# Kernel optimization log

Measured on AMD Instinct MI355X. Metric: run time of the kernel, lower is better.

The kernel has to match this reference:

```python
import jax, jax.numpy as jnp
import numpy as np

DIMENSIONS = 10000
NUM_LEVELS = 100
SIZE = 617
NUM_CLASSES = 26
BATCH = 32


def setup_inputs() -> dict:
    key = jax.random.key(0)
    k1, k2, k3 = jax.random.split(key, 3)
    x = jax.random.uniform(k1, (BATCH, SIZE), dtype=jnp.float32)  # values in [0,1]
    # Random embedding: bipolar {-1,+1} hypervectors
    id_weight = jnp.where(jax.random.uniform(k2, (SIZE, DIMENSIONS)) > 0.5, 1.0, -1.0).astype(jnp.float32)
    # Level embedding: bipolar hypervectors per quantization level
    level_weight = jnp.where(jax.random.uniform(k3, (NUM_LEVELS, DIMENSIONS)) > 0.5, 1.0, -1.0).astype(jnp.float32)
    classify_weight = jnp.zeros((NUM_CLASSES, DIMENSIONS), dtype=jnp.float32)
    return {"x": x, "id_weight": id_weight, "level_weight": level_weight, "classify_weight": classify_weight}


def reference(x, id_weight, level_weight, classify_weight):
    # Level embedding: map continuous values in [low=0, high=1] to level indices
    idx = jnp.clip(jnp.round(x * (NUM_LEVELS - 1)), 0, NUM_LEVELS - 1).astype(jnp.int32)  # (B, S)
    value_hv = level_weight[idx]                     # gather -> (B, S, D)
    bound = id_weight[None, :, :] * value_hv         # bind (elementwise multiply)
    multiset = jnp.sum(bound, axis=1)                # sum over feature axis -> (B, D)
    enc = jnp.where(multiset > 0, 1.0, -1.0)         # hard_quantize
    logit = jnp.einsum('bd,cd->bc', enc, classify_weight)  # Linear, no bias
    return logit
```

## Files before the change

### kernel.cpp

```cpp
#include <hip/hip_runtime.h>

typedef unsigned int u32;
typedef unsigned char u8;
typedef unsigned long long u64;

#define DIMS   10000
#define LEVELS 100
#define SSIZE  617
#define SPAD   624
#define NCLS   26
#define BATCH  32
#define WORDS  313
#define WPITCH 320
#define DPITCH 10240
#define NTILE  5
#define NCH    13
#define CHUNK  48
#define SOPITCH 640

#define OFF_OFFT 0x000000u
#define OFF_IDB  0x020000u
#define OFF_LVB  0x100000u
#define OFF_P8   0x140000u
#define SLOT_BYTES ((size_t)BATCH * DPITCH)

#define PK_ROWS (SPAD + LEVELS + 1)

__global__ __launch_bounds__(256) void k_pack(const float* __restrict__ x,
                                              const float* __restrict__ idw,
                                              const float* __restrict__ lvw,
                                              u32* __restrict__ idb,
                                              u32* __restrict__ lvb,
                                              u32* __restrict__ offt,
                                              float* __restrict__ out)
{
    const int g = blockIdx.x;
    const int r = blockIdx.y;
    const int t = threadIdx.x;
    const bool isLvl = r >= SPAD;
    const int rl = r - SPAD;
    const int d0 = g * 1024 + 4 * t;

    u32 nib = 0;
    const bool rowValid = isLvl ? (rl < LEVELS) : (r < SSIZE);
    if (d0 + 3 < DIMS && rowValid) {
        const float* src = isLvl ? (lvw + (size_t)rl * DIMS)
                                 : (idw + (size_t)r * DIMS);
        float4 f = *(const float4*)(src + d0);
        nib =  (__builtin_bit_cast(u32, f.x) >> 31)
            | ((__builtin_bit_cast(u32, f.y) >> 31) << 1)
            | ((__builtin_bit_cast(u32, f.z) >> 31) << 2)
            | ((__builtin_bit_cast(u32, f.w) >> 31) << 3);
    }
    __shared__ u32 nibs[256];
    nibs[t] = nib;
    __syncthreads();
    if (t < 32) {
        u32 w = 0;
#pragma unroll
        for (int j = 0; j < 8; ++j) w |= nibs[t * 8 + j] << (4 * j);
        u32* dst = isLvl ? (lvb + (size_t)rl * WPITCH)
                         : (idb + (size_t)r * WPITCH);
        dst[g * 32 + t] = w;
    }

    const int B = r * 10 + g;
    const int t2 = B * 256 + t;
    if (t2 < SPAD * BATCH) {
        int s = t2 >> 5, b = t2 & 31;
        u32 off = (u32)LEVELS * WPITCH;
        if (s < SSIZE) {
            float v = x[b * SSIZE + s];
            float rr = rintf(v * (float)(LEVELS - 1));
            int q = (int)rr;
            q = q < 0 ? 0 : (q > LEVELS - 1 ? LEVELS - 1 : q);
            off = (u32)q * WPITCH;
        }
        offt[b * SOPITCH + s] = off;
    }
    if (t2 < BATCH * NCLS) out[t2] = 0.0f;
}

#define CSA6(xv)                                                              \
    {                                                                         \
        u32 car = ones & (xv);                                                \
        ones ^= (xv);                                                         \
        u32 tt;                                                               \
        tt = c0 & car; c0 ^= car; car = tt;                                   \
        tt = c1 & car; c1 ^= car; car = tt;                                   \
        tt = c2 & car; c2 ^= car; car = tt;                                   \
        tt = c3 & car; c3 ^= car; car = tt;                                   \
        c4 ^= car;                                                            \
    }

__device__ __forceinline__ void spread6_1(u32* __restrict__ part,
                                          int slot, int b, int wq,
                                          u32 ones, u32 c0, u32 c1,
                                          u32 c2, u32 c3, u32 c4)
{
    u32* dst = part + ((size_t)(slot * BATCH + b) * DPITCH + (size_t)wq * 32) / 4;
    u32 o[8];
#pragma unroll
    for (int g = 0; g < 8; ++g) {
        int sh = 4 * g;
        u32 n;
        n  =  (((ones >> sh) & 0xFu) * 0x00204081u) & 0x01010101u;
        n |= ((((c0   >> sh) & 0xFu) * 0x00204081u) & 0x01010101u) << 1;
        n |= ((((c1   >> sh) & 0xFu) * 0x00204081u) & 0x01010101u) << 2;
        n |= ((((c2   >> sh) & 0xFu) * 0x00204081u) & 0x01010101u) << 3;
        n |= ((((c3   >> sh) & 0xFu) * 0x00204081u) & 0x01010101u) << 4;
        n |= ((((c4   >> sh) & 0xFu) * 0x01010101u) & 0x01010101u) << 5;
        o[g] = n;
    }
#pragma unroll
    for (int g = 0; g < 8; ++g) {
        int sh = 4 * g;
        u32 n;
        n  =  (((ones >> sh) & 0xFu) * 0x00204081u) & 0x01010101u;
        n |= ((((c0   >> sh) & 0xFu) * 0x00204081u) & 0x01010101u) << 1;
        n |= ((((c1   >> sh) & 0xFu) * 0x00204081u) & 0x01010101u) << 2;
        n |= ((((c2   >> sh) & 0xFu) * 0x00204081u) & 0x01010101u) << 3;
        n |= ((((c3   >> sh) & 0xFu) * 0x00204081u) & 0x01010101u) << 4;
        n |= ((((c4   >> sh) & 0xFu) * 0x00204081u) & 0x01010101u) << 5;
        o[g] = n;
    }
    *(uint4*)(dst)     = make_uint4(o[0], o[1], o[2], o[3]);
    *(uint4*)(dst + 4) = make_uint4(o[4], o[5], o[6], o[7]);
}

template <int CH>
__global__ __launch_bounds__(64) void k_bind_t(const u32* __restrict__ idb,
                                               const u32* __restrict__ lvb,
                                               const u32* __restrict__ offt,
                                               u32* __restrict__ part)
{
    const int wq   = blockIdx.x * 64 + threadIdx.x;
    const int b    = blockIdx.y;
    const int slot = blockIdx.z;
    const int sBeg = slot * CH;

    u32 off[CH];
#pragma unroll
    for (int k = 0; k < CH; ++k) off[k] = offt[b * SOPITCH + sBeg + k];

    u32 ones = 0, c0 = 0, c1 = 0, c2 = 0, c3 = 0, c4 = 0;

#pragma unroll
    for (int grp = 0; grp < CH / 16; ++grp) {
        u32 u[16], l[16];
#pragma unroll
        for (int k = 0; k < 16; ++k) {
            const int s = sBeg + grp * 16 + k;
            u[k] = idb[(size_t)s * WPITCH + wq];
            l[k] = lvb[off[grp * 16 + k] + wq];
        }
#pragma unroll
        for (int k = 0; k < 16; ++k) {
            u32 xv = u[k] ^ l[k];
            CSA6(xv);
        }
    }
    spread6_1(part, slot, b, wq, ones, c0, c1, c2, c3, c4);
}

__global__ __launch_bounds__(64) void k_bind_g(const u32* __restrict__ idb,
                                               const u32* __restrict__ lvb,
                                               const u32* __restrict__ offt,
                                               u32* __restrict__ part,
                                               int chunk)
{
    const int wq   = blockIdx.x * 64 + threadIdx.x;
    const int b    = blockIdx.y;
    const int slot = blockIdx.z;
    const int sBeg = slot * chunk;
    const int sEnd = min(SPAD, sBeg + chunk);

    u32 ones = 0, c0 = 0, c1 = 0, c2 = 0, c3 = 0, c4 = 0;
    for (int s = sBeg; s < sEnd; ++s) {
        u32 u1 = idb[(size_t)s * WPITCH + wq];
        u32 l1 = lvb[offt[b * SOPITCH + s] + wq];
        u32 xv = u1 ^ l1;
        CSA6(xv);
    }
    spread6_1(part, slot, b, wq, ones, c0, c1, c2, c3, c4);
}

template <int NCHT>
__global__ __launch_bounds__(256) void k_encl_t(const u32* __restrict__ part,
                                                const float* __restrict__ W,
                                                float* __restrict__ out)
{
    const int b = blockIdx.y;
    const int q = blockIdx.x;
    const int t = threadIdx.x;
    const int dw = q * 256 + t;
    const u32* p = part + (size_t)b * (DPITCH / 4) + dw;
    const size_t cs = (size_t)BATCH * (DPITCH / 4);

    u32 v[NCHT];
#pragma unroll
    for (int c = 0; c < NCHT; ++c) v[c] = p[(size_t)c * cs];
    u32 a01 = 0, a23 = 0;
#pragma unroll
    for (int c = 0; c < NCHT; ++c) {
        a01 += v[c] & 0x00FF00FFu;
        a23 += (v[c] >> 8) & 0x00FF00FFu;
    }
    const float e0 = (int)(a01 & 0xFFFFu) <= 308 ? 1.0f : -1.0f;
    const float e1 = (int)(a23 & 0xFFFFu) <= 308 ? 1.0f : -1.0f;
    const float e2 = (int)(a01 >> 16)     <= 308 ? 1.0f : -1.0f;
    const float e3 = (int)(a23 >> 16)     <= 308 ? 1.0f : -1.0f;

    float acc[NCLS];
    if (dw < DIMS / 4) {
#pragma unroll
        for (int cc = 0; cc < NCLS; ++cc) {
            float4 w4 = *(const float4*)(W + (size_t)cc * DIMS + 4 * dw);
            acc[cc] = fmaf(e0, w4.x, fmaf(e1, w4.y, fmaf(e2, w4.z, e3 * w4.w)));
        }
    } else {
#pragma unroll
        for (int cc = 0; cc < NCLS; ++cc) acc[cc] = 0.0f;
    }

#pragma unroll
    for (int cc = 0; cc < NCLS; ++cc) {
#pragma unroll
        for (int o = 32; o > 0; o >>= 1)
            acc[cc] += __shfl_xor(acc[cc], o);
    }
    __shared__ float red[4][NCLS];
    const int lane = t & 63, wv = t >> 6;
    if (lane == 0) {
#pragma unroll
        for (int cc = 0; cc < NCLS; ++cc) red[wv][cc] = acc[cc];
    }
    __syncthreads();
    if (t < NCLS) {
        float vv = red[0][t] + red[1][t] + red[2][t] + red[3][t];
        atomicAdd(out + b * NCLS + t, vv);
    }
}

__global__ __launch_bounds__(256) void k_encl_g(const u32* __restrict__ part,
                                                const float* __restrict__ W,
                                                float* __restrict__ out,
                                                int nch)
{
    const int b = blockIdx.y;
    const int q = blockIdx.x;
    const int t = threadIdx.x;
    const int dw = q * 256 + t;
    const u32* p = part + (size_t)b * (DPITCH / 4) + dw;
    const size_t cs = (size_t)BATCH * (DPITCH / 4);
    u32 a01 = 0, a23 = 0;
    for (int c = 0; c < nch; ++c) {
        u32 v = p[(size_t)c * cs];
        a01 += v & 0x00FF00FFu;
        a23 += (v >> 8) & 0x00FF00FFu;
    }
    const float e0 = (int)(a01 & 0xFFFFu) <= 308 ? 1.0f : -1.0f;
    const float e1 = (int)(a23 & 0xFFFFu) <= 308 ? 1.0f : -1.0f;
    const float e2 = (int)(a01 >> 16)     <= 308 ? 1.0f : -1.0f;
    const float e3 = (int)(a23 >> 16)     <= 308 ? 1.0f : -1.0f;
    float acc[NCLS];
    if (dw < DIMS / 4) {
#pragma unroll
        for (int cc = 0; cc < NCLS; ++cc) {
            float4 w4 = *(const float4*)(W + (size_t)cc * DIMS + 4 * dw);
            acc[cc] = fmaf(e0, w4.x, fmaf(e1, w4.y, fmaf(e2, w4.z, e3 * w4.w)));
        }
    } else {
#pragma unroll
        for (int cc = 0; cc < NCLS; ++cc) acc[cc] = 0.0f;
    }
#pragma unroll
    for (int cc = 0; cc < NCLS; ++cc) {
#pragma unroll
        for (int o = 32; o > 0; o >>= 1)
            acc[cc] += __shfl_xor(acc[cc], o);
    }
    __shared__ float red[4][NCLS];
    const int lane = t & 63, wv = t >> 6;
    if (lane == 0) {
#pragma unroll
        for (int cc = 0; cc < NCLS; ++cc) red[wv][cc] = acc[cc];
    }
    __syncthreads();
    if (t < NCLS) {
        float vv = red[0][t] + red[1][t] + red[2][t] + red[3][t];
        atomicAdd(out + b * NCLS + t, vv);
    }
}

extern "C" void kernel_launch(void* const* d_in, const int* in_sizes, int n_in,
                              void* d_out, int out_size, void* d_ws, size_t ws_size,
                              hipStream_t stream)
{
    const float* x   = (const float*)d_in[0];
    const float* idw = (const float*)d_in[1];
    const float* lvw = (const float*)d_in[2];
    const float* W   = (const float*)d_in[3];
    float* out = (float*)d_out;

    char* ws = (char*)d_ws;
    u32* offt = (u32*)(ws + OFF_OFFT);
    u32* idb  = (u32*)(ws + OFF_IDB);
    u32* lvb  = (u32*)(ws + OFF_LVB);
    u32* part = (u32*)(ws + OFF_P8);

    size_t avail = ws_size > OFF_P8 ? ws_size - OFF_P8 : 0;
    const bool fast = avail >= (size_t)NCH * SLOT_BYTES;

    dim3 g1(10, PK_ROWS);
    k_pack<<<g1, 256, 0, stream>>>(x, idw, lvw, idb, lvb, offt, out);

    if (fast) {
        dim3 g2(NTILE, BATCH, NCH);
        k_bind_t<CHUNK><<<g2, 64, 0, stream>>>(idb, lvb, offt, part);
        dim3 g3(10, BATCH);
        k_encl_t<NCH><<<g3, 256, 0, stream>>>(part, W, out);
    } else {
        int nch = (int)(avail / SLOT_BYTES);
        if (nch < 1) nch = 1;
        int chunk = (SPAD + nch - 1) / nch;
        if (chunk > 62) chunk = 62;
        nch = (SPAD + chunk - 1) / chunk;
        dim3 g2(NTILE, BATCH, nch);
        k_bind_g<<<g2, 64, 0, stream>>>(idb, lvb, offt, part, chunk);
        dim3 g3(10, BATCH);
        k_encl_g<<<g3, 256, 0, stream>>>(part, W, out, nch);
    }
}
```

Before: 91.00 us.

## Stage level bit-tiles in LDS, halve chunk size and narrow counters

The bind kernel now uses 256-thread blocks that cover four batch rows. Each block first stages a 64-word slice of all level hypervectors (plus a zero pad row) in shared memory, so the level gathers read LDS instead of global memory. The chunk shrinks to 24 features across 26 slots, which lets the carry-save counter drop from 6 bits to 5 and removes the duplicated spread loop. The cost is that the reduction kernel must combine twice as many partial slots, plus a per-block LDS fill of about 25KB. The offset table is rescaled to the LDS row stride, and the fallback path decodes it back to the global pitch.

```diff
diff --git a/kernel.cpp b/kernel.cpp
--- a/kernel.cpp
+++ b/kernel.cpp
@@ -14,8 +14,8 @@
 #define WPITCH 320
 #define DPITCH 10240
 #define NTILE  5
-#define NCH    13
-#define CHUNK  48
+#define NCH    26
+#define CHUNK  24
 #define SOPITCH 640
 
 #define OFF_OFFT 0x000000u
@@ -68,20 +68,20 @@
     const int t2 = B * 256 + t;
     if (t2 < SPAD * BATCH) {
         int s = t2 >> 5, b = t2 & 31;
-        u32 off = (u32)LEVELS * WPITCH;
+        u32 off = (u32)LEVELS * 256u;
         if (s < SSIZE) {
             float v = x[b * SSIZE + s];
             float rr = rintf(v * (float)(LEVELS - 1));
             int q = (int)rr;
             q = q < 0 ? 0 : (q > LEVELS - 1 ? LEVELS - 1 : q);
-            off = (u32)q * WPITCH;
+            off = (u32)q * 256u;
         }
         offt[b * SOPITCH + s] = off;
     }
     if (t2 < BATCH * NCLS) out[t2] = 0.0f;
 }
 
-#define CSA6(xv)                                                              \
+#define CSA5(xv)                                                              \
     {                                                                         \
         u32 car = ones & (xv);                                                \
         ones ^= (xv);                                                         \
@@ -89,14 +89,13 @@
         tt = c0 & car; c0 ^= car; car = tt;                                   \
         tt = c1 & car; c1 ^= car; car = tt;                                   \
         tt = c2 & car; c2 ^= car; car = tt;                                   \
-        tt = c3 & car; c3 ^= car; car = tt;                                   \
-        c4 ^= car;                                                            \
-    }
-
-__device__ __forceinline__ void spread6_1(u32* __restrict__ part,
-                                          int slot, int b, int wq,
-                                          u32 ones, u32 c0, u32 c1,
-                                          u32 c2, u32 c3, u32 c4)
+        c3 ^= car;                                                            \
+    }
+
+__device__ __forceinline__ void spread5(u32* __restrict__ part,
+                                        int slot, int b, int wq,
+                                        u32 ones, u32 c0, u32 c1,
+                                        u32 c2, u32 c3)
 {
     u32* dst = part + ((size_t)(slot * BATCH + b) * DPITCH + (size_t)wq * 32) / 4;
     u32 o[8];
@@ -109,19 +108,6 @@
         n |= ((((c1   >> sh) & 0xFu) * 0x00204081u) & 0x01010101u) << 2;
         n |= ((((c2   >> sh) & 0xFu) * 0x00204081u) & 0x01010101u) << 3;
         n |= ((((c3   >> sh) & 0xFu) * 0x00204081u) & 0x01010101u) << 4;
-        n |= ((((c4   >> sh) & 0xFu) * 0x01010101u) & 0x01010101u) << 5;
-        o[g] = n;
-    }
-#pragma unroll
-    for (int g = 0; g < 8; ++g) {
-        int sh = 4 * g;
-        u32 n;
-        n  =  (((ones >> sh) & 0xFu) * 0x00204081u) & 0x01010101u;
-        n |= ((((c0   >> sh) & 0xFu) * 0x00204081u) & 0x01010101u) << 1;
-        n |= ((((c1   >> sh) & 0xFu) * 0x00204081u) & 0x01010101u) << 2;
-        n |= ((((c2   >> sh) & 0xFu) * 0x00204081u) & 0x01010101u) << 3;
-        n |= ((((c3   >> sh) & 0xFu) * 0x00204081u) & 0x01010101u) << 4;
-        n |= ((((c4   >> sh) & 0xFu) * 0x00204081u) & 0x01010101u) << 5;
         o[g] = n;
     }
     *(uint4*)(dst)     = make_uint4(o[0], o[1], o[2], o[3]);
@@ -129,13 +115,31 @@
 }
 
 template <int CH>
-__global__ __launch_bounds__(64) void k_bind_t(const u32* __restrict__ idb,
-                                               const u32* __restrict__ lvb,
-                                               const u32* __restrict__ offt,
-                                               u32* __restrict__ part)
-{
-    const int wq   = blockIdx.x * 64 + threadIdx.x;
-    const int b    = blockIdx.y;
+__global__ __launch_bounds__(256) void k_bind_t(const u32* __restrict__ idb,
+                                                const u32* __restrict__ lvb,
+                                                const u32* __restrict__ offt,
+                                                u32* __restrict__ part)
+{
+    __shared__ u32 tile[(LEVELS + 1) * 64];
+    const int tid = threadIdx.x;
+    const int W0 = blockIdx.x * 64;
+
+    {
+        u32 stg[25];
+#pragma unroll
+        for (int k = 0; k < 25; ++k) {
+            int idx = k * 256 + tid;
+            stg[k] = lvb[(size_t)(idx >> 6) * WPITCH + W0 + (idx & 63)];
+        }
+#pragma unroll
+        for (int k = 0; k < 25; ++k) tile[k * 256 + tid] = stg[k];
+        if (tid < 64) tile[6400 + tid] = 0;
+    }
+    __syncthreads();
+
+    const int lane = tid & 63;
+    const int wq = W0 + lane;
+    const int b = __builtin_amdgcn_readfirstlane(blockIdx.y * 4 + (tid >> 6));
     const int slot = blockIdx.z;
     const int sBeg = slot * CH;
 
@@ -143,24 +147,15 @@
 #pragma unroll
     for (int k = 0; k < CH; ++k) off[k] = offt[b * SOPITCH + sBeg + k];
 
-    u32 ones = 0, c0 = 0, c1 = 0, c2 = 0, c3 = 0, c4 = 0;
-
-#pragma unroll
-    for (int grp = 0; grp < CH / 16; ++grp) {
-        u32 u[16], l[16];
-#pragma unroll
-        for (int k = 0; k < 16; ++k) {
-            const int s = sBeg + grp * 16 + k;
-            u[k] = idb[(size_t)s * WPITCH + wq];
-            l[k] = lvb[off[grp * 16 + k] + wq];
-        }
-#pragma unroll
-        for (int k = 0; k < 16; ++k) {
-            u32 xv = u[k] ^ l[k];
-            CSA6(xv);
-        }
-    }
-    spread6_1(part, slot, b, wq, ones, c0, c1, c2, c3, c4);
+    u32 ones = 0, c0 = 0, c1 = 0, c2 = 0, c3 = 0;
+#pragma unroll
+    for (int k = 0; k < CH; ++k) {
+        u32 u = idb[(size_t)(sBeg + k) * WPITCH + wq];
+        u32 l = tile[(off[k] >> 2) + lane];
+        u32 xv = u ^ l;
+        CSA5(xv);
+    }
+    spread5(part, slot, b, wq, ones, c0, c1, c2, c3);
 }
 
 __global__ __launch_bounds__(64) void k_bind_g(const u32* __restrict__ idb,
@@ -175,14 +170,15 @@
     const int sBeg = slot * chunk;
     const int sEnd = min(SPAD, sBeg + chunk);
 
-    u32 ones = 0, c0 = 0, c1 = 0, c2 = 0, c3 = 0, c4 = 0;
+    u32 ones = 0, c0 = 0, c1 = 0, c2 = 0, c3 = 0;
     for (int s = sBeg; s < sEnd; ++s) {
         u32 u1 = idb[(size_t)s * WPITCH + wq];
-        u32 l1 = lvb[offt[b * SOPITCH + s] + wq];
+        u32 q  = offt[b * SOPITCH + s] >> 8;
+        u32 l1 = lvb[(size_t)q * WPITCH + wq];
         u32 xv = u1 ^ l1;
-        CSA6(xv);
-    }
-    spread6_1(part, slot, b, wq, ones, c0, c1, c2, c3, c4);
+        CSA5(xv);
+    }
+    spread5(part, slot, b, wq, ones, c0, c1, c2, c3);
 }
 
 template <int NCHT>
@@ -316,15 +312,15 @@
     k_pack<<<g1, 256, 0, stream>>>(x, idw, lvw, idb, lvb, offt, out);
 
     if (fast) {
-        dim3 g2(NTILE, BATCH, NCH);
-        k_bind_t<CHUNK><<<g2, 64, 0, stream>>>(idb, lvb, offt, part);
+        dim3 g2(NTILE, 8, NCH);
+        k_bind_t<CHUNK><<<g2, 256, 0, stream>>>(idb, lvb, offt, part);
         dim3 g3(10, BATCH);
         k_encl_t<NCH><<<g3, 256, 0, stream>>>(part, W, out);
     } else {
         int nch = (int)(avail / SLOT_BYTES);
         if (nch < 1) nch = 1;
         int chunk = (SPAD + nch - 1) / nch;
-        if (chunk > 62) chunk = 62;
+        if (chunk > 31) chunk = 31;
         nch = (SPAD + chunk - 1) / chunk;
         dim3 g2(NTILE, BATCH, nch);
         k_bind_g<<<g2, 64, 0, stream>>>(idb, lvb, offt, part, chunk);
```

After: 93.18 us. 2.4% more time.
